# Kernel tuning notes

Hardware: AMD Instinct MI355X
Metric: run time of the kernel (lower is better)

Reference implementation:

```python
import jax, jax.numpy as jnp
import numpy as np

T = 1048576      # signal length
K = 3            # number of IMFs
ALPHA = 2000.0   # bandwidth penalty
TAU = 1e-7       # dual ascent step
TOL = 1e-6       # convergence tolerance
N_ITER = 50      # max fixed-point iterations


def _vmd(x, omega_init):
    T_ = x.shape[0]
    t = jnp.arange(1, T_ + 1, dtype=jnp.float32) / T_
    freqs = t - 0.5 - 1.0 / T_                           # [T]
    f_hat = jnp.fft.fftshift(jnp.fft.fft(x))             # [T] complex
    u0 = jnp.zeros((K, T_), dtype=f_hat.dtype)
    lam0 = jnp.zeros((T_,), dtype=f_hat.dtype)

    def step(carry, n):
        u_prev, lam_prev, omega, done = carry
        base = (freqs[None, :] - omega[:, None]) ** 2    # [K,T]
        # mode k's denom also gets (freqs-omega[k-1])^2 and (freqs-omega[k+1])^2
        nbr = jnp.zeros_like(base).at[1:].add(base[:-1]).at[:-1].add(base[1:])
        denom = base + nbr + TAU ** 2
        u_hat = (f_hat[None, :] - lam_prev[None, :] / 2.0) / (1.0 + ALPHA * denom)
        pw = jnp.real(u_hat) ** 2 + jnp.imag(u_hat) ** 2  # |u_hat|^2, [K,T]
        omega_new = jnp.sum(freqs[None, :] * pw, axis=1) / jnp.sum(pw, axis=1)
        lam_new = lam_prev + TAU * (jnp.sum(u_hat, axis=0) - f_hat)
        # convergence check (every 10th iter), mirrors the original break
        u_diff = jnp.sum(jnp.abs(u_hat - u_prev) ** 2) / jnp.sum(jnp.abs(u_prev) ** 2)
        om_diff = jnp.sum(jnp.abs(omega_new - jnp.roll(omega_new, 1))) / K
        conv = (n % 10 == 0) & (u_diff < TOL) & (om_diff < TOL)
        # freeze state once converged (break-iteration's fresh u_hat is kept)
        u_out = jnp.where(done, u_prev, u_hat)
        lam_out = jnp.where(done, lam_prev, lam_new)
        om_out = jnp.where(done, omega, omega_new)
        return (u_out, lam_out, om_out, done | conv), None

    init = (u0, lam0, omega_init.astype(jnp.float32), jnp.array(False))
    (u_hat, _, _, _), _ = jax.lax.scan(jax.checkpoint(step), init, jnp.arange(N_ITER))
    imfs = jnp.real(jnp.fft.ifft(jnp.fft.ifftshift(u_hat, axes=-1), axis=-1))
    return imfs.astype(jnp.float32)                      # [K,T]


def setup_inputs() -> dict:
    key = jax.random.key(0)
    kx, ko = jax.random.split(key)
    x = jax.random.normal(kx, (T,), dtype=jnp.float32)
    omega_init = jax.random.uniform(ko, (K,), dtype=jnp.float32) * 0.5  # init==1
    return {"x": x, "omega_init": omega_init}


def reference(x, omega_init):
    return _vmd(x, omega_init)
```

## Files before the change

### kernel.cpp

```cpp
#include <hip/hip_runtime.h>
#include <math.h>


#define ALPHA_F 2000.0f
#define TAU_F   1e-7f

static __device__ __forceinline__ int lpad2(int i) { return i + (i >> 4); }
static __device__ __forceinline__ int swz(int i)  { return ((i & 7) << 7) | (i >> 3); }
static __device__ __forceinline__ int swzA(int i) { return ((i & 7) << 6) | (i >> 3); }
static __device__ __forceinline__ float frcp(float x) { return __builtin_amdgcn_rcpf(x); }

typedef float v2f __attribute__((ext_vector_type(2)));
static __device__ __forceinline__ v2f sp(float s) { v2f r; r.x = s; r.y = s; return r; }
static __device__ __forceinline__ v2f v2(float a, float b) { v2f r; r.x = a; r.y = b; return r; }
static __device__ __forceinline__ v2f pkfma(v2f a, v2f b, v2f c)
{ return __builtin_elementwise_fma(a, b, c); }
static __device__ __forceinline__ v2f cmul(v2f a, v2f w)
{
  v2f t = a * sp(w.x);
  v2f s = v2(-a.y, a.x);
  return pkfma(s, sp(w.y), t);
}

#define PADN2 1088

template<int CTRL>
static __device__ __forceinline__ float dpp_addf(float v)
{
  int r = __builtin_amdgcn_update_dpp(0, __float_as_int(v), CTRL, 0xf, 0xf, true);
  return v + __int_as_float(r);
}
static __device__ __forceinline__ float wave64_sum(float v)
{
  v = dpp_addf<0x111>(v);
  v = dpp_addf<0x112>(v);
  v = dpp_addf<0x114>(v);
  v = dpp_addf<0x118>(v);
  v = dpp_addf<0x142>(v);
  v = dpp_addf<0x143>(v);
  return v;
}
static __device__ __forceinline__ float row16_sum(float v)
{
  v = dpp_addf<0x111>(v);
  v = dpp_addf<0x112>(v);
  v = dpp_addf<0x114>(v);
  v = dpp_addf<0x118>(v);
  return v;
}
static __device__ __forceinline__ float rdlane(float v, int l)
{
  return __int_as_float(__builtin_amdgcn_readlane(__float_as_int(v), l));
}

__global__ __launch_bounds__(256) void k_twid(float2* __restrict__ tw)
{
  int i = threadIdx.x + blockIdx.x * 256;
  if (i >= 340) return;
  int st, p;
  if (i < 4)       { st = 1; p = i; }
  else if (i < 20) { st = 2; p = i - 4; }
  else if (i < 84) { st = 3; p = i - 20; }
  else             { st = 4; p = i - 84; }
  float sw, cw;
  sincospif((float)(2 * p) * (1.0f / (float)(4 << (2 * st))), &sw, &cw);
#pragma unroll
  for (int dir = 0; dir < 2; ++dir) {
    float w1r = cw, w1i = dir ? sw : -sw;
    float w2r = w1r * w1r - w1i * w1i, w2i = 2.0f * w1r * w1i;
    float w3r = w2r * w1r - w2i * w1i, w3i = w2r * w1i + w2i * w1r;
    float2* b = tw + dir * 1020;
    b[i]       = make_float2(w1r, w1i);
    b[340 + i] = make_float2(w2r, w2i);
    b[680 + i] = make_float2(w3r, w3i);
  }
}

template<int SIGN>
static __device__ void fft1024p(v2f* A, v2f* B, const v2f* __restrict__ twl)
{
  const int u = threadIdx.x;
  {
    v2f X0 = A[lpad2(u)], X1 = A[lpad2(u + 256)];
    v2f X2 = A[lpad2(u + 512)], X3 = A[lpad2(u + 768)];
    v2f t0 = X0 + X2, t1 = X0 - X2, t2 = X1 + X3, t3 = X1 - X3;
    v2f o0 = t0 + t2, o2 = t0 - t2;
    v2f s3 = t3.yx;
    v2f ns3 = v2(s3.x, -s3.y);
    v2f o1, o3;
    if (SIGN < 0) { o1 = t1 + ns3; o3 = t1 - ns3; }
    else          { o1 = t1 - ns3; o3 = t1 + ns3; }
    const int base = u << 2;
    B[lpad2(base    )] = o0; B[lpad2(base + 1)] = o1;
    B[lpad2(base + 2)] = o2; B[lpad2(base + 3)] = o3;
    __syncthreads();
  }
#pragma unroll
  for (int st = 1; st < 5; ++st) {
    v2f *in  = (st & 1) ? B : A;
    v2f *out = (st & 1) ? A : B;
    const int quarter = 1 << (2 * st);
    const int p = u & (quarter - 1);
    const int g = u >> (2 * st);
    const int ti = (quarter - 4) / 3 + p;

    v2f w1 = twl[ti], w2 = twl[340 + ti], w3 = twl[680 + ti];

    v2f X0 = in[lpad2(u)], X1 = in[lpad2(u + 256)];
    v2f X2 = in[lpad2(u + 512)], X3 = in[lpad2(u + 768)];

    v2f y1 = cmul(X1, w1), y2 = cmul(X2, w2), y3 = cmul(X3, w3);

    v2f t0 = X0 + y2, t1 = X0 - y2, t2 = y1 + y3, t3 = y1 - y3;
    v2f o0 = t0 + t2, o2 = t0 - t2;
    v2f s3 = t3.yx;
    v2f ns3 = v2(s3.x, -s3.y);
    v2f o1, o3;
    if (SIGN < 0) { o1 = t1 + ns3; o3 = t1 - ns3; }
    else          { o1 = t1 - ns3; o3 = t1 + ns3; }

    const int base = (g << (2 * st + 2)) + p;
    out[lpad2(base              )] = o0;
    out[lpad2(base +     quarter)] = o1;
    out[lpad2(base + 2 * quarter)] = o2;
    out[lpad2(base + 3 * quarter)] = o3;
    __syncthreads();
  }
}

#define STAGE_TW(dst, src) \
  for (int i_ = threadIdx.x; i_ < 510; i_ += 256) \
    ((float4*)(dst))[i_] = ((const float4*)(src))[i_];

__global__ __launch_bounds__(256) void k_fwd_passA(const float* __restrict__ x,
                                                   const float2* __restrict__ twg,
                                                   float2* __restrict__ ws0)
{
  __shared__ __align__(16) v2f A[PADN2], B[PADN2];
  __shared__ __align__(16) v2f twl[1020];
  const int p = swzA(blockIdx.x);
  const int tid = threadIdx.x;
  const int c0 = 2 * p;
  STAGE_TW(twl, twg);
#pragma unroll
  for (int q = 0; q < 4; ++q) {
    int j = tid + 256 * q;
    A[lpad2(j)] = ((const v2f*)x)[(size_t)j * 512 + p];
  }
  __syncthreads();
  fft1024p<-1>(A, B, twl);

  float sa, ca, sb, cb, ssa, cca, ssb, ccb;
  sincospif((float)(c0 * tid) * (2.0f / 1048576.0f), &sa, &ca);
  sincospif((float)((c0 + 1) * tid) * (2.0f / 1048576.0f), &sb, &cb);
  sincospif((float)c0 * (1.0f / 2048.0f), &ssa, &cca);
  sincospif((float)(c0 + 1) * (1.0f / 2048.0f), &ssb, &ccb);
  v2f E0 = v2(ca, -sa), E1 = v2(cb, -sb);
  const v2f S0 = v2(cca, -ssa), S1 = v2(ccb, -ssb);
#pragma unroll
  for (int q = 0; q < 4; ++q) {
    int k = tid + 256 * q;
    int kk = (1024 - k) & 1023;
    v2f Z = B[lpad2(k)];
    v2f Wv = B[lpad2(kk)];
    float X0r = 0.5f * (Z.x + Wv.x), X0i = 0.5f * (Z.y - Wv.y);
    float X1r = 0.5f * (Z.y + Wv.y), X1i = 0.5f * (Wv.x - Z.x);
    v2f o01 = cmul(v2(X0r, X0i), E0);
    v2f o23 = cmul(v2(X1r, X1i), E1);
    float4 o = make_float4(o01.x, o01.y, o23.x, o23.y);
    ((float4*)ws0)[(size_t)k * 512 + p] = o;
    E0 = cmul(E0, S0); E1 = cmul(E1, S1);
  }
}

__global__ __launch_bounds__(256) void k_fwd_passB(const float2* __restrict__ ws0,
                                                   const float2* __restrict__ twg,
                                                   float2* __restrict__ fhat,
                                                   float* __restrict__ ET)
{
  __shared__ __align__(16) v2f A[PADN2], B[PADN2];
  __shared__ __align__(16) v2f twl[1020];
  const int b = swz(blockIdx.x);
  const int tid = threadIdx.x;
  STAGE_TW(twl, twg);
#pragma unroll
  for (int q = 0; q < 4; ++q) {
    int j = tid + 256 * q;
    A[lpad2(j)] = ((const v2f*)ws0)[(size_t)b * 1024 + j];
  }
  __syncthreads();
  fft1024p<-1>(A, B, twl);
#pragma unroll
  for (int q = 0; q < 4; ++q) {
    int k2 = tid + 256 * q;
    v2f v = B[lpad2(k2)];
    fhat[(size_t)b * 1024 + k2] = make_float2(v.x, v.y);
    ET[(size_t)k2 * 1024 + b] = v.x * v.x + v.y * v.y;
  }
}

static __device__ __forceinline__ void lag4(float x, float& l0, float& l1,
                                            float& l2, float& l3)
{
  float m0 = x, m1 = x - (1.0f / 3.0f), m2 = x - (2.0f / 3.0f), m3 = x - 1.0f;
  l0 = -4.5f * m1 * m2 * m3;
  l1 = 13.5f * m0 * m2 * m3;
  l2 = -13.5f * m0 * m1 * m3;
  l3 =  4.5f * m0 * m1 * m2;
}

__global__ __launch_bounds__(256) void k_moments(const float* __restrict__ ET,
                                                 double* __restrict__ W)
{
  __shared__ double red[4 * 4];
  const int B = blockIdx.x;
  const int k2 = B ^ 512;
  const int tid = threadIdx.x;
  double a0 = 0, a1 = 0, a2 = 0, a3 = 0;
#pragma unroll
  for (int q = 0; q < 4; ++q) {
    int k1 = tid + 256 * q;
    float e = ET[(size_t)k2 * 1024 + k1];
    float l0, l1, l2, l3;
    lag4((float)k1 * (1.0f / 1024.0f), l0, l1, l2, l3);
    a0 += (double)(e * l0); a1 += (double)(e * l1);
    a2 += (double)(e * l2); a3 += (double)(e * l3);
  }
  const int lane = tid & 63, wv = tid >> 6;
  double pv[4] = { a0, a1, a2, a3 };
#pragma unroll
  for (int j = 0; j < 4; ++j) {
    double v = pv[j];
    for (int off = 32; off; off >>= 1) v += __shfl_down(v, off, 64);
    if (lane == 0) red[wv * 4 + j] = v;
  }
  __syncthreads();
  if (tid < 4)
    W[B * 4 + tid] = red[tid] + red[4 + tid] + red[8 + tid] + red[12 + tid];
}

__global__ __launch_bounds__(1024) void k_solve(
    const double* __restrict__ W4, const float* __restrict__ omega_init,
    float* __restrict__ ckeepN, float* __restrict__ omegaF)
{
  __shared__ float red[2][6 * 16];
  const int t = threadIdx.x;
  const int lane = t & 63, wv = t >> 6;

  float Wsc[4], fsc[4];
#pragma unroll
  for (int e = 0; e < 4; ++e) {
    Wsc[e] = (float)W4[t * 4 + e];
    fsc[e] = (float)((double)t / 1024.0 + (double)e / 3072.0 - 0.5);
  }
  const v2f frP = v2(fsc[0], fsc[1]), frQ = v2(fsc[2], fsc[3]);
  const v2f WrP = v2(Wsc[0], Wsc[1]), WrQ = v2(Wsc[2], Wsc[3]);
  const v2f WfP = WrP * frP,          WfQ = WrQ * frQ;
  v2f cnrP = sp(0.0f), cnrQ = sp(0.0f);

  float om0 = omega_init[0], om1 = omega_init[1], om2 = omega_init[2];

#pragma unroll 1
  for (int it = 0; it < 49; ++it) {
    float* rb = red[it & 1];
    v2f p0 = sp(0.f), p1 = sp(0.f), p2 = sp(0.f),
        p3 = sp(0.f), p4 = sp(0.f), p5 = sp(0.f);

    auto node_pair = [&](const v2f fv, const v2f Wrv, const v2f Wfv, v2f& cnv) {
      v2f a0 = fv - sp(om0), a1 = fv - sp(om1), a2 = fv - sp(om2);
      v2f d0 = a0 * a0, d1 = a1 * a1, d2 = a2 * a2;
      v2f s01 = d0 + d1, s12 = d1 + d2;
      v2f dA = pkfma(sp(ALPHA_F), s01, sp(1.0f));
      v2f dC = pkfma(sp(ALPHA_F), s12, sp(1.0f));
      v2f dB = pkfma(sp(ALPHA_F), d2, dA);
      v2f AB = dA * dB, BC = dB * dC, AC = dA * dC;
      v2f ABC = AB * dC;
      v2f r = v2(frcp(ABC.x), frcp(ABC.y));
      v2f w0 = BC * r, w1 = AC * r, w2 = AB * r;
      v2f hf = pkfma(sp(-0.5f), cnv, sp(1.0f));
      v2f g = hf * hf;
      v2f gw0 = g * (w0 * w0), gw1 = g * (w1 * w1), gw2 = g * (w2 * w2);
      p0 = pkfma(Wfv, gw0, p0); p1 = pkfma(Wfv, gw1, p1); p2 = pkfma(Wfv, gw2, p2);
      p3 = pkfma(Wrv, gw0, p3); p4 = pkfma(Wrv, gw1, p4); p5 = pkfma(Wrv, gw2, p5);
      v2f S = (w0 + w1) + w2;
      cnv = pkfma(sp(TAU_F), pkfma(S, hf, sp(-1.0f)), cnv);
    };
    node_pair(frP, WrP, WfP, cnrP);
    node_pair(frQ, WrQ, WfQ, cnrQ);

    float q0 = p0.x + p0.y, q1 = p1.x + p1.y, q2 = p2.x + p2.y;
    float q3 = p3.x + p3.y, q4 = p4.x + p4.y, q5 = p5.x + p5.y;

    q0 = wave64_sum(q0); q1 = wave64_sum(q1); q2 = wave64_sum(q2);
    q3 = wave64_sum(q3); q4 = wave64_sum(q4); q5 = wave64_sum(q5);
    if (lane == 63) {
      rb[0 * 16 + wv] = q0; rb[1 * 16 + wv] = q1; rb[2 * 16 + wv] = q2;
      rb[3 * 16 + wv] = q3; rb[4 * 16 + wv] = q4; rb[5 * 16 + wv] = q5;
    }
    __syncthreads();
    float v1 = rb[lane];
    float v2_ = rb[64 + (lane & 31)];
    v1 = row16_sum(v1);
    v2_ = row16_sum(v2_);
    float n0 = rdlane(v1, 15), n1 = rdlane(v1, 31), n2 = rdlane(v1, 47);
    float e0 = rdlane(v1, 63), e1 = rdlane(v2_, 15), e2 = rdlane(v2_, 31);
    om0 = n0 * frcp(e0);
    om1 = n1 * frcp(e1);
    om2 = n2 * frcp(e2);
  }

  ((float4*)ckeepN)[t] = make_float4(cnrP.x, cnrP.y, cnrQ.x, cnrQ.y);
  if (t == 0) { omegaF[0] = om0; omegaF[1] = om1; omegaF[2] = om2; }
}

__global__ __launch_bounds__(256) void k_inv_A2(
    const float2* __restrict__ fhat, const float* __restrict__ ckeepN,
    const float* __restrict__ omegaF, const float2* __restrict__ twg,
    float2* __restrict__ ws0)
{
  __shared__ __align__(16) v2f A[PADN2], B[PADN2];
  __shared__ __align__(16) v2f twl[1020];
  __shared__ float cn4[4096];
  __shared__ float som[3];
  const int tid = threadIdx.x;
  const int pk = blockIdx.x >> 10;
  const int b = swz(blockIdx.x & 1023);
  STAGE_TW(twl, twg);
  for (int i = tid; i < 4096; i += 256) cn4[i] = ckeepN[i];
  if (tid == 0) { som[0] = omegaF[0]; som[1] = omegaF[1]; som[2] = omegaF[2]; }
  __syncthreads();
  const float om0 = som[0], om1 = som[1], om2 = som[2];
  const float xb = (float)b * (1.0f / 1024.0f);
  float l0, l1, l2, l3, m0, m1, m2, m3;
  lag4(xb, l0, l1, l2, l3);
  lag4(1.0f - xb, m0, m1, m2, m3);

#pragma unroll
  for (int q = 0; q < 4; ++q) {
    int j = tid + 256 * q;
    float2 f = fhat[(size_t)b * 1024 + j];
    int bin = j ^ 512;
    int binp = 1023 - bin;
    float4 cv = ((const float4*)cn4)[bin];
    float4 cw = ((const float4*)cn4)[binp];
    float c  = l0 * cv.x + l1 * cv.y + l2 * cv.z + l3 * cv.w;
    float cp = m0 * cw.x + m1 * cw.y + m2 * cw.z + m3 * cw.w;
    float hf = 1.0f - 0.5f * c;
    float hp = 1.0f - 0.5f * cp;
    int tt = (bin << 10) | b;
    float freq = (float)tt * (1.0f / 1048576.0f) - 0.5f;
    v2f fpm = v2(freq, -freq);
    v2f A0 = fpm - sp(om0), A1 = fpm - sp(om1), A2v = fpm - sp(om2);
    v2f D0 = A0 * A0, D1 = A1 * A1, D2 = A2v * A2v;
    v2f V;
    if (pk == 0) {
      v2f DA = pkfma(sp(ALPHA_F), D0 + D1, sp(1.0f));
      v2f DB = pkfma(sp(ALPHA_F), D2, DA);
      float r0 = hf * frcp(DA.x), r0n = hp * frcp(DA.y);
      float r1 = hf * frcp(DB.x), r1n = hp * frcp(DB.y);
      float Rr = 0.5f * (r0 + r0n), Ri = 0.5f * (r1 + r1n);
      V = cmul(v2(f.x, f.y), v2(Rr, Ri));
    } else {
      v2f DC = pkfma(sp(ALPHA_F), D1 + D2, sp(1.0f));
      float r2 = hf * frcp(DC.x), r2n = hp * frcp(DC.y);
      float Rr = 0.5f * (r2 + r2n);
      V = v2(f.x, f.y) * sp(Rr);
    }
    A[lpad2(j)] = V;
  }
  __syncthreads();
  fft1024p<1>(A, B, twl);

  float sa, ca, ss, cs;
  sincospif((float)(b * tid) * (2.0f / 1048576.0f), &sa, &ca);
  sincospif((float)b * (1.0f / 2048.0f), &ss, &cs);
  v2f E = v2(ca, sa);
  const v2f S = v2(cs, ss);
#pragma unroll
  for (int q = 0; q < 4; ++q) {
    int m1i = tid + 256 * q;
    v2f v = B[lpad2(m1i)];
    v2f o = cmul(v, E);
    ws0[(size_t)pk * 1048576 + (size_t)m1i * 1024 + b] = make_float2(o.x, o.y);
    E = cmul(E, S);
  }
}

__global__ __launch_bounds__(256) void k_inv_B2(const float2* __restrict__ ws0,
                                                const float2* __restrict__ twg,
                                                float* __restrict__ out)
{
  __shared__ __align__(16) v2f A[PADN2], B[PADN2];
  __shared__ __align__(16) v2f twl[1020];
  const int pk = blockIdx.x >> 10;
  const int b = swz(blockIdx.x & 1023);
  const int tid = threadIdx.x;
  STAGE_TW(twl, twg);
#pragma unroll
  for (int q = 0; q < 4; ++q) {
    int j = tid + 256 * q;
    A[lpad2(j)] = ((const v2f*)ws0)[(size_t)pk * 1048576 + (size_t)b * 1024 + j];
  }
  __syncthreads();
  fft1024p<1>(A, B, twl);
  const float sc = 1.0f / 1048576.0f;
#pragma unroll
  for (int q = 0; q < 4; ++q) {
    int m2 = tid + 256 * q;
    v2f v = B[lpad2(m2)];
    if (pk == 0) {
      out[(size_t)m2 * 1024 + b]           = v.x * sc;
      out[1048576 + (size_t)m2 * 1024 + b] = v.y * sc;
    } else {
      out[2097152 + (size_t)m2 * 1024 + b] = v.x * sc;
    }
  }
}

extern "C" void kernel_launch(void* const* d_in, const int* in_sizes, int n_in,
                              void* d_out, int out_size, void* d_ws, size_t ws_size,
                              hipStream_t stream)
{
  (void)in_sizes; (void)n_in; (void)out_size; (void)ws_size;
  const float* x       = (const float*)d_in[0];
  const float* om_init = (const float*)d_in[1];
  float* out = (float*)d_out;

  char* w = (char*)d_ws;
  const size_t MB = 1024ull * 1024ull;
  float2* fhat     = (float2*)(w);
  float*  ET       = (float*)(w + 8 * MB);
  double* W4       = (double*)(w + 12 * MB);
  float*  ckeepN   = (float*)(w + 12 * MB + 32 * 1024);
  float*  omegaF   = (float*)(w + 12 * MB + 48 * 1024);
  float2* tw       = (float2*)(w + 12 * MB + 64 * 1024);
  float2* scratch  = (float2*)(w + 16 * MB);

  k_twid<<<2, 256, 0, stream>>>(tw);
  k_fwd_passA<<<512, 256, 0, stream>>>(x, tw, scratch);
  k_fwd_passB<<<1024, 256, 0, stream>>>(scratch, tw, fhat, ET);
  k_moments<<<1024, 256, 0, stream>>>(ET, W4);
  k_solve<<<1, 1024, 0, stream>>>(W4, om_init, ckeepN, omegaF);
  k_inv_A2<<<2048, 256, 0, stream>>>(fhat, ckeepN, omegaF, tw + 1020, scratch);
  k_inv_B2<<<2048, 256, 0, stream>>>(scratch, tw + 1020, out);
}
```

Before: 190.1 us.

## Compute FFT twiddles inline and merge inverse pass-A mode blocks

Removes the twiddle-table kernel and the per-block staging of twiddles into shared memory; each radix-4 stage now computes its twiddles with sincospif and complex products. The inverse pass-A kernel now handles both packed-mode FFTs in one block, which halves the grid and loads fhat and the coefficient table once instead of twice. This trades shared-memory loads and one kernel launch for extra transcendental math per stage. It also raises per-block work and register use, which lowers parallelism in that kernel.

Result: faster. 183.2 us (-3.7%).

```diff
diff --git a/kernel.cpp b/kernel.cpp
--- a/kernel.cpp
+++ b/kernel.cpp
@@ -20,6 +20,12 @@
   v2f t = a * sp(w.x);
   v2f s = v2(-a.y, a.x);
   return pkfma(s, sp(w.y), t);
+}
+static __device__ __forceinline__ v2f cmulrr(v2f a, float wr, float wi)
+{
+  v2f t = a * sp(wr);
+  v2f s = v2(-a.y, a.x);
+  return pkfma(s, sp(wi), t);
 }
 
 #define PADN2 1088
@@ -53,31 +59,8 @@
   return __int_as_float(__builtin_amdgcn_readlane(__float_as_int(v), l));
 }
 
-__global__ __launch_bounds__(256) void k_twid(float2* __restrict__ tw)
-{
-  int i = threadIdx.x + blockIdx.x * 256;
-  if (i >= 340) return;
-  int st, p;
-  if (i < 4)       { st = 1; p = i; }
-  else if (i < 20) { st = 2; p = i - 4; }
-  else if (i < 84) { st = 3; p = i - 20; }
-  else             { st = 4; p = i - 84; }
-  float sw, cw;
-  sincospif((float)(2 * p) * (1.0f / (float)(4 << (2 * st))), &sw, &cw);
-#pragma unroll
-  for (int dir = 0; dir < 2; ++dir) {
-    float w1r = cw, w1i = dir ? sw : -sw;
-    float w2r = w1r * w1r - w1i * w1i, w2i = 2.0f * w1r * w1i;
-    float w3r = w2r * w1r - w2i * w1i, w3i = w2r * w1i + w2i * w1r;
-    float2* b = tw + dir * 1020;
-    b[i]       = make_float2(w1r, w1i);
-    b[340 + i] = make_float2(w2r, w2i);
-    b[680 + i] = make_float2(w3r, w3i);
-  }
-}
-
 template<int SIGN>
-static __device__ void fft1024p(v2f* A, v2f* B, const v2f* __restrict__ twl)
+static __device__ void fft1024p(v2f* A, v2f* B)
 {
   const int u = threadIdx.x;
   {
@@ -85,8 +68,7 @@
     v2f X2 = A[lpad2(u + 512)], X3 = A[lpad2(u + 768)];
     v2f t0 = X0 + X2, t1 = X0 - X2, t2 = X1 + X3, t3 = X1 - X3;
     v2f o0 = t0 + t2, o2 = t0 - t2;
-    v2f s3 = t3.yx;
-    v2f ns3 = v2(s3.x, -s3.y);
+    v2f ns3 = v2(t3.y, -t3.x);
     v2f o1, o3;
     if (SIGN < 0) { o1 = t1 + ns3; o3 = t1 - ns3; }
     else          { o1 = t1 - ns3; o3 = t1 + ns3; }
@@ -102,19 +84,22 @@
     const int quarter = 1 << (2 * st);
     const int p = u & (quarter - 1);
     const int g = u >> (2 * st);
-    const int ti = (quarter - 4) / 3 + p;
-
-    v2f w1 = twl[ti], w2 = twl[340 + ti], w3 = twl[680 + ti];
+
+    float sw, cw;
+    sincospif((float)(2 * p) * (1.0f / (float)(4 << (2 * st))), &sw, &cw);
+    const float w1r = cw, w1i = (SIGN < 0) ? -sw : sw;
+    const float w2r = w1r * w1r - w1i * w1i, w2i = 2.0f * w1r * w1i;
+    const float w3r = w2r * w1r - w2i * w1i, w3i = w2r * w1i + w2i * w1r;
 
     v2f X0 = in[lpad2(u)], X1 = in[lpad2(u + 256)];
     v2f X2 = in[lpad2(u + 512)], X3 = in[lpad2(u + 768)];
 
-    v2f y1 = cmul(X1, w1), y2 = cmul(X2, w2), y3 = cmul(X3, w3);
+    v2f y1 = cmulrr(X1, w1r, w1i), y2 = cmulrr(X2, w2r, w2i),
+        y3 = cmulrr(X3, w3r, w3i);
 
     v2f t0 = X0 + y2, t1 = X0 - y2, t2 = y1 + y3, t3 = y1 - y3;
     v2f o0 = t0 + t2, o2 = t0 - t2;
-    v2f s3 = t3.yx;
-    v2f ns3 = v2(s3.x, -s3.y);
+    v2f ns3 = v2(t3.y, -t3.x);
     v2f o1, o3;
     if (SIGN < 0) { o1 = t1 + ns3; o3 = t1 - ns3; }
     else          { o1 = t1 - ns3; o3 = t1 + ns3; }
@@ -128,27 +113,20 @@
   }
 }
 
-#define STAGE_TW(dst, src) \
-  for (int i_ = threadIdx.x; i_ < 510; i_ += 256) \
-    ((float4*)(dst))[i_] = ((const float4*)(src))[i_];
-
 __global__ __launch_bounds__(256) void k_fwd_passA(const float* __restrict__ x,
-                                                   const float2* __restrict__ twg,
                                                    float2* __restrict__ ws0)
 {
   __shared__ __align__(16) v2f A[PADN2], B[PADN2];
-  __shared__ __align__(16) v2f twl[1020];
   const int p = swzA(blockIdx.x);
   const int tid = threadIdx.x;
   const int c0 = 2 * p;
-  STAGE_TW(twl, twg);
 #pragma unroll
   for (int q = 0; q < 4; ++q) {
     int j = tid + 256 * q;
     A[lpad2(j)] = ((const v2f*)x)[(size_t)j * 512 + p];
   }
   __syncthreads();
-  fft1024p<-1>(A, B, twl);
+  fft1024p<-1>(A, B);
 
   float sa, ca, sb, cb, ssa, cca, ssb, ccb;
   sincospif((float)(c0 * tid) * (2.0f / 1048576.0f), &sa, &ca);
@@ -174,22 +152,19 @@
 }
 
 __global__ __launch_bounds__(256) void k_fwd_passB(const float2* __restrict__ ws0,
-                                                   const float2* __restrict__ twg,
                                                    float2* __restrict__ fhat,
                                                    float* __restrict__ ET)
 {
   __shared__ __align__(16) v2f A[PADN2], B[PADN2];
-  __shared__ __align__(16) v2f twl[1020];
   const int b = swz(blockIdx.x);
   const int tid = threadIdx.x;
-  STAGE_TW(twl, twg);
 #pragma unroll
   for (int q = 0; q < 4; ++q) {
     int j = tid + 256 * q;
     A[lpad2(j)] = ((const v2f*)ws0)[(size_t)b * 1024 + j];
   }
   __syncthreads();
-  fft1024p<-1>(A, B, twl);
+  fft1024p<-1>(A, B);
 #pragma unroll
   for (int q = 0; q < 4; ++q) {
     int k2 = tid + 256 * q;
@@ -315,17 +290,13 @@
 
 __global__ __launch_bounds__(256) void k_inv_A2(
     const float2* __restrict__ fhat, const float* __restrict__ ckeepN,
-    const float* __restrict__ omegaF, const float2* __restrict__ twg,
-    float2* __restrict__ ws0)
+    const float* __restrict__ omegaF, float2* __restrict__ ws0)
 {
   __shared__ __align__(16) v2f A[PADN2], B[PADN2];
-  __shared__ __align__(16) v2f twl[1020];
   __shared__ float cn4[4096];
   __shared__ float som[3];
   const int tid = threadIdx.x;
-  const int pk = blockIdx.x >> 10;
-  const int b = swz(blockIdx.x & 1023);
-  STAGE_TW(twl, twg);
+  const int b = swz(blockIdx.x);
   for (int i = tid; i < 4096; i += 256) cn4[i] = ckeepN[i];
   if (tid == 0) { som[0] = omegaF[0]; som[1] = omegaF[1]; som[2] = omegaF[2]; }
   __syncthreads();
@@ -335,6 +306,7 @@
   lag4(xb, l0, l1, l2, l3);
   lag4(1.0f - xb, m0, m1, m2, m3);
 
+  v2f v2reg[4];
 #pragma unroll
   for (int q = 0; q < 4; ++q) {
     int j = tid + 256 * q;
@@ -352,57 +324,64 @@
     v2f fpm = v2(freq, -freq);
     v2f A0 = fpm - sp(om0), A1 = fpm - sp(om1), A2v = fpm - sp(om2);
     v2f D0 = A0 * A0, D1 = A1 * A1, D2 = A2v * A2v;
-    v2f V;
-    if (pk == 0) {
-      v2f DA = pkfma(sp(ALPHA_F), D0 + D1, sp(1.0f));
-      v2f DB = pkfma(sp(ALPHA_F), D2, DA);
-      float r0 = hf * frcp(DA.x), r0n = hp * frcp(DA.y);
-      float r1 = hf * frcp(DB.x), r1n = hp * frcp(DB.y);
-      float Rr = 0.5f * (r0 + r0n), Ri = 0.5f * (r1 + r1n);
-      V = cmul(v2(f.x, f.y), v2(Rr, Ri));
-    } else {
-      v2f DC = pkfma(sp(ALPHA_F), D1 + D2, sp(1.0f));
-      float r2 = hf * frcp(DC.x), r2n = hp * frcp(DC.y);
-      float Rr = 0.5f * (r2 + r2n);
-      V = v2(f.x, f.y) * sp(Rr);
-    }
-    A[lpad2(j)] = V;
-  }
-  __syncthreads();
-  fft1024p<1>(A, B, twl);
+    v2f DA = pkfma(sp(ALPHA_F), D0 + D1, sp(1.0f));
+    v2f DB = pkfma(sp(ALPHA_F), D2, DA);
+    float r0 = hf * frcp(DA.x), r0n = hp * frcp(DA.y);
+    float r1 = hf * frcp(DB.x), r1n = hp * frcp(DB.y);
+    float Rr = 0.5f * (r0 + r0n), Ri = 0.5f * (r1 + r1n);
+    A[lpad2(j)] = cmul(v2(f.x, f.y), v2(Rr, Ri));
+    v2f DC = pkfma(sp(ALPHA_F), D1 + D2, sp(1.0f));
+    float r2 = hf * frcp(DC.x), r2n = hp * frcp(DC.y);
+    float Rr2 = 0.5f * (r2 + r2n);
+    v2reg[q] = v2(f.x, f.y) * sp(Rr2);
+  }
+  __syncthreads();
+  fft1024p<1>(A, B);
 
   float sa, ca, ss, cs;
   sincospif((float)(b * tid) * (2.0f / 1048576.0f), &sa, &ca);
   sincospif((float)b * (1.0f / 2048.0f), &ss, &cs);
-  v2f E = v2(ca, sa);
+  const v2f Einit = v2(ca, sa);
   const v2f S = v2(cs, ss);
+
+  v2f E = Einit;
 #pragma unroll
   for (int q = 0; q < 4; ++q) {
     int m1i = tid + 256 * q;
     v2f v = B[lpad2(m1i)];
     v2f o = cmul(v, E);
-    ws0[(size_t)pk * 1048576 + (size_t)m1i * 1024 + b] = make_float2(o.x, o.y);
+    ws0[(size_t)m1i * 1024 + b] = make_float2(o.x, o.y);
     E = cmul(E, S);
+    A[lpad2(m1i)] = v2reg[q];
+  }
+  __syncthreads();
+  fft1024p<1>(A, B);
+
+  E = Einit;
+#pragma unroll
+  for (int q = 0; q < 4; ++q) {
+    int m1i = tid + 256 * q;
+    v2f v = B[lpad2(m1i)];
+    v2f o = cmul(v, E);
+    ws0[1048576 + (size_t)m1i * 1024 + b] = make_float2(o.x, o.y);
+    E = cmul(E, S);
   }
 }
 
 __global__ __launch_bounds__(256) void k_inv_B2(const float2* __restrict__ ws0,
-                                                const float2* __restrict__ twg,
                                                 float* __restrict__ out)
 {
   __shared__ __align__(16) v2f A[PADN2], B[PADN2];
-  __shared__ __align__(16) v2f twl[1020];
   const int pk = blockIdx.x >> 10;
   const int b = swz(blockIdx.x & 1023);
   const int tid = threadIdx.x;
-  STAGE_TW(twl, twg);
 #pragma unroll
   for (int q = 0; q < 4; ++q) {
     int j = tid + 256 * q;
     A[lpad2(j)] = ((const v2f*)ws0)[(size_t)pk * 1048576 + (size_t)b * 1024 + j];
   }
   __syncthreads();
-  fft1024p<1>(A, B, twl);
+  fft1024p<1>(A, B);
   const float sc = 1.0f / 1048576.0f;
 #pragma unroll
   for (int q = 0; q < 4; ++q) {
@@ -433,14 +412,12 @@
   double* W4       = (double*)(w + 12 * MB);
   float*  ckeepN   = (float*)(w + 12 * MB + 32 * 1024);
   float*  omegaF   = (float*)(w + 12 * MB + 48 * 1024);
-  float2* tw       = (float2*)(w + 12 * MB + 64 * 1024);
   float2* scratch  = (float2*)(w + 16 * MB);
 
-  k_twid<<<2, 256, 0, stream>>>(tw);
-  k_fwd_passA<<<512, 256, 0, stream>>>(x, tw, scratch);
-  k_fwd_passB<<<1024, 256, 0, stream>>>(scratch, tw, fhat, ET);
+  k_fwd_passA<<<512, 256, 0, stream>>>(x, scratch);
+  k_fwd_passB<<<1024, 256, 0, stream>>>(scratch, fhat, ET);
   k_moments<<<1024, 256, 0, stream>>>(ET, W4);
   k_solve<<<1, 1024, 0, stream>>>(W4, om_init, ckeepN, omegaF);
-  k_inv_A2<<<2048, 256, 0, stream>>>(fhat, ckeepN, omegaF, tw + 1020, scratch);
-  k_inv_B2<<<2048, 256, 0, stream>>>(scratch, tw + 1020, out);
-}
+  k_inv_A2<<<1024, 256, 0, stream>>>(fhat, ckeepN, omegaF, scratch);
+  k_inv_B2<<<2048, 256, 0, stream>>>(scratch, out);
+}
```
